# Optimization experiments

Measured on AMD Instinct MI355X. Metric: run time of the kernel, lower is better.

The kernel has to match this reference:

```python
import jax, jax.numpy as jnp
import numpy as np

D_MODEL = 1024
NUM_HEADS = 16
DEPTH = D_MODEL // NUM_HEADS
B, S = 2, 2048


def setup_inputs() -> dict:
    key = jax.random.key(0)
    ks = jax.random.split(key, 13)
    sc = 1.0 / np.sqrt(D_MODEL)
    inp = {
        "q": jax.random.normal(ks[0], (B, S, D_MODEL), jnp.float32),
        "k": jax.random.normal(ks[1], (B, S, D_MODEL), jnp.float32),
        "v": jax.random.normal(ks[2], (B, S, D_MODEL), jnp.float32),
        "mask": jax.random.randint(ks[3], (B, 1, S, S), 0, 2).astype(jnp.float32),
        "wq": jax.random.normal(ks[4], (D_MODEL, D_MODEL), jnp.float32) * sc,
        "bq": jnp.zeros((D_MODEL,), jnp.float32),
        "wk": jax.random.normal(ks[5], (D_MODEL, D_MODEL), jnp.float32) * sc,
        "bk": jnp.zeros((D_MODEL,), jnp.float32),
        "wv": jax.random.normal(ks[6], (D_MODEL, D_MODEL), jnp.float32) * sc,
        "bv": jnp.zeros((D_MODEL,), jnp.float32),
        "wo": jax.random.normal(ks[7], (D_MODEL, D_MODEL), jnp.float32) * sc,
        "bo": jnp.zeros((D_MODEL,), jnp.float32),
    }
    return inp


def _split_heads(x):
    # [B,S,D] -> [B,H,S,depth]
    b, s, _ = x.shape
    return x.reshape(b, s, NUM_HEADS, DEPTH).transpose(0, 2, 1, 3)


def reference(q, k, v, mask, wq, bq, wk, bk, wv, bv, wo, bo):
    qh = _split_heads(q @ wq.T + bq)
    kh = _split_heads(k @ wk.T + bk)
    vh = _split_heads(v @ wv.T + bv)
    logits = jnp.einsum("bhqd,bhkd->bhqk", qh, kh) / jnp.sqrt(
        jnp.asarray(DEPTH, jnp.float32))
    logits = logits + mask * (-1e9)
    attn = jax.nn.softmax(logits, axis=-1)
    out = jnp.einsum("bhqk,bhkd->bhqd", attn, vh)
    out = out.transpose(0, 2, 1, 3).reshape(q.shape[0], -1, D_MODEL)
    return out @ wo.T + bo
```

## Files before the change

kernel.cpp:

```cpp
#include <hip/hip_runtime.h>

#define D_MODEL 1024
#define NHEADS  16
#define DEPTH   64
#define BATCH   2
#define SEQ     2048
#define MROWS   (BATCH * SEQ)

typedef unsigned short u16;
typedef unsigned int   u32;
typedef unsigned long long u64;
typedef __bf16 bf16x8 __attribute__((ext_vector_type(8)));
typedef float  f32x4  __attribute__((ext_vector_type(4)));

__device__ __forceinline__ u16 f2b(float f) {
    return __builtin_bit_cast(u16, static_cast<__bf16>(f));
}
__device__ __forceinline__ bf16x8 ldb8(const u16* p) {
    return __builtin_bit_cast(bf16x8, *(const uint4*)p);
}

__global__ __launch_bounds__(256) void pack_mask(
    const float* __restrict__ mask, u64* __restrict__ bits)
{
    const int w    = blockIdx.x * 4 + (threadIdx.x >> 6);
    const int lane = threadIdx.x & 63;
    float m = mask[(size_t)w * 64 + lane];
    u64 b = __ballot(m > 0.5f);
    if (lane == 0) bits[w] = b;
}

__global__ __launch_bounds__(256, 3) void proj3(
    const float* __restrict__ q, const float* __restrict__ k, const float* __restrict__ v,
    const float* __restrict__ wq, const float* __restrict__ wk, const float* __restrict__ wv,
    const float* __restrict__ bq, const float* __restrict__ bk, const float* __restrict__ bv,
    u16* __restrict__ qws, u16* __restrict__ kws, u16* __restrict__ vtws)
{
    __shared__ __align__(16) u16 ldsA[128 * 40];
    __shared__ __align__(16) u16 ldsB[128 * 40];

    const int z = blockIdx.z;
    const float* X  = (z == 0) ? q  : (z == 1) ? k  : v;
    const float* W  = (z == 0) ? wq : (z == 1) ? wk : wv;
    const float* Bi = (z == 0) ? bq : (z == 1) ? bk : bv;
    u16* dst        = (z == 0) ? qws : (z == 1) ? kws : vtws;

    const int tid  = threadIdx.x;
    const int wv_  = tid >> 6;
    const int lane = tid & 63;
    const int quad = lane >> 4;
    const int l15  = lane & 15;
    const int bx = blockIdx.x, by = blockIdx.y;
    const int wm = (wv_ >> 1) * 64;
    const int wn = (wv_ & 1) * 64;

    f32x4 acc[4][4];
    for (int i = 0; i < 4; ++i)
        for (int j = 0; j < 4; ++j)
            acc[i][j] = (f32x4){0.f, 0.f, 0.f, 0.f};

    const int rowA0 = by * 128;
    const int rowB0 = bx * 128;

    const int sr = tid >> 3;
    const int sc = (tid & 7) * 4;

    float4 pa[4], pb[4];
    #pragma unroll
    for (int i = 0; i < 4; ++i) {
        pa[i] = *(const float4*)&X[(size_t)(rowA0 + sr + i * 32) * D_MODEL + sc];
        pb[i] = *(const float4*)&W[(size_t)(rowB0 + sr + i * 32) * D_MODEL + sc];
    }

    for (int it = 0; it < 32; ++it) {
        #pragma unroll
        for (int i = 0; i < 4; ++i) {
            ushort4 ha, hb;
            ha.x = f2b(pa[i].x); ha.y = f2b(pa[i].y); ha.z = f2b(pa[i].z); ha.w = f2b(pa[i].w);
            hb.x = f2b(pb[i].x); hb.y = f2b(pb[i].y); hb.z = f2b(pb[i].z); hb.w = f2b(pb[i].w);
            *(ushort4*)&ldsA[(sr + i * 32) * 40 + sc] = ha;
            *(ushort4*)&ldsB[(sr + i * 32) * 40 + sc] = hb;
        }
        __syncthreads();

        if (it < 31) {
            const int k0 = (it + 1) * 32;
            #pragma unroll
            for (int i = 0; i < 4; ++i) {
                pa[i] = *(const float4*)&X[(size_t)(rowA0 + sr + i * 32) * D_MODEL + k0 + sc];
                pb[i] = *(const float4*)&W[(size_t)(rowB0 + sr + i * 32) * D_MODEL + k0 + sc];
            }
        }

        bf16x8 af[4], bfr[4];
        #pragma unroll
        for (int t = 0; t < 4; ++t) {
            af[t]  = ldb8(&ldsA[(wm + t * 16 + l15) * 40 + quad * 8]);
            bfr[t] = ldb8(&ldsB[(wn + t * 16 + l15) * 40 + quad * 8]);
        }
        #pragma unroll
        for (int mt = 0; mt < 4; ++mt)
            #pragma unroll
            for (int nt = 0; nt < 4; ++nt)
                acc[mt][nt] = __builtin_amdgcn_mfma_f32_16x16x32_bf16(af[mt], bfr[nt], acc[mt][nt], 0, 0, 0);
        __syncthreads();
    }

    #pragma unroll
    for (int nt = 0; nt < 4; ++nt) {
        int n = bx * 128 + wn + nt * 16 + l15;
        float bvv = Bi[n];
        int h = n >> 6, d = n & 63;
        #pragma unroll
        for (int mt = 0; mt < 4; ++mt) {
            #pragma unroll
            for (int r = 0; r < 4; ++r) {
                int m = by * 128 + wm + mt * 16 + quad * 4 + r;
                float c = acc[mt][nt][r] + bvv;
                int b = m >> 11, s = m & (SEQ - 1);
                if (z != 2)
                    dst[(((size_t)(b * NHEADS + h) * SEQ) + s) * DEPTH + d] = f2b(c);
                else
                    dst[(((size_t)(b * NHEADS + h) * DEPTH) + d) * SEQ + s] = f2b(c);
            }
        }
    }
}

__global__ __launch_bounds__(256) void gemm_out(
    const u16* __restrict__ X, const float* __restrict__ W,
    const float* __restrict__ bias, float* __restrict__ out)
{
    __shared__ __align__(16) u16 ldsA[128 * 40];
    __shared__ __align__(16) u16 ldsB[64 * 40];

    const int tid  = threadIdx.x;
    const int wv_  = tid >> 6;
    const int lane = tid & 63;
    const int quad = lane >> 4;
    const int l15  = lane & 15;
    const int bx = blockIdx.x, by = blockIdx.y;
    const int wm = (wv_ >> 1) * 64;
    const int wn = (wv_ & 1) * 32;

    f32x4 acc[4][2];
    for (int i = 0; i < 4; ++i)
        for (int j = 0; j < 2; ++j)
            acc[i][j] = (f32x4){0.f, 0.f, 0.f, 0.f};

    const int rowA0 = by * 128;
    const int rowB0 = bx * 64;

    const int ar = tid >> 2, akc = (tid & 3) * 8;
    const int br = tid >> 3, bc = (tid & 7) * 4;

    uint4  paA[2];
    float4 paB[2];
    #pragma unroll
    for (int i = 0; i < 2; ++i) {
        paA[i] = *(const uint4*)&X[(size_t)(rowA0 + ar + i * 64) * D_MODEL + akc];
        paB[i] = *(const float4*)&W[(size_t)(rowB0 + br + i * 32) * D_MODEL + bc];
    }

    for (int it = 0; it < 32; ++it) {
        #pragma unroll
        for (int i = 0; i < 2; ++i) {
            *(uint4*)&ldsA[(ar + i * 64) * 40 + akc] = paA[i];
            ushort4 hb;
            hb.x = f2b(paB[i].x); hb.y = f2b(paB[i].y); hb.z = f2b(paB[i].z); hb.w = f2b(paB[i].w);
            *(ushort4*)&ldsB[(br + i * 32) * 40 + bc] = hb;
        }
        __syncthreads();

        if (it < 31) {
            const int k0 = (it + 1) * 32;
            #pragma unroll
            for (int i = 0; i < 2; ++i) {
                paA[i] = *(const uint4*)&X[(size_t)(rowA0 + ar + i * 64) * D_MODEL + k0 + akc];
                paB[i] = *(const float4*)&W[(size_t)(rowB0 + br + i * 32) * D_MODEL + k0 + bc];
            }
        }

        bf16x8 af[4], bfr[2];
        #pragma unroll
        for (int t = 0; t < 4; ++t)
            af[t] = ldb8(&ldsA[(wm + t * 16 + l15) * 40 + quad * 8]);
        #pragma unroll
        for (int t = 0; t < 2; ++t)
            bfr[t] = ldb8(&ldsB[(wn + t * 16 + l15) * 40 + quad * 8]);
        #pragma unroll
        for (int mt = 0; mt < 4; ++mt)
            #pragma unroll
            for (int nt = 0; nt < 2; ++nt)
                acc[mt][nt] = __builtin_amdgcn_mfma_f32_16x16x32_bf16(af[mt], bfr[nt], acc[mt][nt], 0, 0, 0);
        __syncthreads();
    }

    #pragma unroll
    for (int nt = 0; nt < 2; ++nt) {
        int n = bx * 64 + wn + nt * 16 + l15;
        float bvv = bias[n];
        #pragma unroll
        for (int mt = 0; mt < 4; ++mt) {
            #pragma unroll
            for (int r = 0; r < 4; ++r) {
                int m = by * 128 + wm + mt * 16 + quad * 4 + r;
                out[(size_t)m * D_MODEL + n] = acc[mt][nt][r] + bvv;
            }
        }
    }
}

__global__ __launch_bounds__(256, 3) void flash_attn(
    const u16* __restrict__ Q, const u16* __restrict__ K,
    const u16* __restrict__ Vt, const u64* __restrict__ maskbits,
    u16* __restrict__ O)
{
    __shared__ __align__(16) u16 ldsK[2][64 * 64];
    __shared__ __align__(16) u16 ldsV[2][64 * 64];
    __shared__ __align__(16) u16 ldsP[4][16 * 72];

    const int tid  = threadIdx.x;
    const int wv_  = tid >> 6;
    const int lane = tid & 63;
    const int quad = lane >> 4;
    const int l15  = lane & 15;
    const int bh = blockIdx.y;
    const int b  = bh >> 4, h = bh & 15;
    const int q0 = blockIdx.x * 64 + wv_ * 16;

    const u16* Qb = Q  + (size_t)bh * SEQ * DEPTH;
    const u16* Kb = K  + (size_t)bh * SEQ * DEPTH;
    const u16* Vb = Vt + (size_t)bh * DEPTH * SEQ;
    const u64* MB = maskbits + (size_t)b * SEQ * (SEQ / 64);

    const int srow = tid >> 3;
    const int sc8  = tid & 7;
    const int swz  = ((sc8 ^ (srow & 7)) * 8);
    const int kdst0 = srow * 64 + swz;
    const int kdst1 = (srow + 32) * 64 + swz;

    const int xk0 = ((quad ^ (l15 & 7)) * 8);
    const int xk1 = (((4 + quad) ^ (l15 & 7)) * 8);

    bf16x8 aq0 = ldb8(&Qb[(q0 + l15) * DEPTH + quad * 8]);
    bf16x8 aq1 = ldb8(&Qb[(q0 + l15) * DEPTH + 32 + quad * 8]);

    f32x4 oa[4];
    for (int i = 0; i < 4; ++i) oa[i] = (f32x4){0.f, 0.f, 0.f, 0.f};
    float lrow[4] = {0.f, 0.f, 0.f, 0.f};

    u16* myP = ldsP[wv_];

    uint4 kreg0 = *(const uint4*)&Kb[(size_t)srow * DEPTH + sc8 * 8];
    uint4 kreg1 = *(const uint4*)&Kb[(size_t)(srow + 32) * DEPTH + sc8 * 8];
    uint4 vreg0 = *(const uint4*)&Vb[(size_t)srow * SEQ + sc8 * 8];
    uint4 vreg1 = *(const uint4*)&Vb[(size_t)(srow + 32) * SEQ + sc8 * 8];

    for (int it = 0; it < 32; ++it) {
        const int buf = it & 1;
        u16* Kl = ldsK[buf];
        u16* Vl = ldsV[buf];

        *(uint4*)&Kl[kdst0] = kreg0;
        *(uint4*)&Kl[kdst1] = kreg1;
        *(uint4*)&Vl[kdst0] = vreg0;
        *(uint4*)&Vl[kdst1] = vreg1;
        __syncthreads();

        if (it < 31) {
            const int kb2 = (it + 1) * 64;
            kreg0 = *(const uint4*)&Kb[(size_t)(kb2 + srow) * DEPTH + sc8 * 8];
            kreg1 = *(const uint4*)&Kb[(size_t)(kb2 + srow + 32) * DEPTH + sc8 * 8];
            vreg0 = *(const uint4*)&Vb[(size_t)srow * SEQ + kb2 + sc8 * 8];
            vreg1 = *(const uint4*)&Vb[(size_t)(srow + 32) * SEQ + kb2 + sc8 * 8];
        }

        u64 mrow[4];
        #pragma unroll
        for (int r = 0; r < 4; ++r)
            mrow[r] = MB[(size_t)(q0 + quad * 4 + r) * (SEQ / 64) + it];

        #pragma unroll
        for (int cc = 0; cc < 4; ++cc) {
            const int row = cc * 16 + l15;
            bf16x8 bk0 = ldb8(&Kl[row * 64 + xk0]);
            bf16x8 bk1 = ldb8(&Kl[row * 64 + xk1]);
            f32x4 z = (f32x4){0.f, 0.f, 0.f, 0.f};
            z = __builtin_amdgcn_mfma_f32_16x16x32_bf16(aq0, bk0, z, 0, 0, 0);
            z = __builtin_amdgcn_mfma_f32_16x16x32_bf16(aq1, bk1, z, 0, 0, 0);
            #pragma unroll
            for (int r = 0; r < 4; ++r) {
                float e = __expf(z[r] * 0.125f);
                float p = ((mrow[r] >> (cc * 16 + l15)) & 1ull) ? 0.f : e;
                lrow[r] += p;
                myP[(quad * 4 + r) * 72 + cc * 16 + l15] = f2b(p);
            }
        }

        __builtin_amdgcn_wave_barrier();
        __builtin_amdgcn_s_waitcnt(0xc07f);
        __builtin_amdgcn_wave_barrier();
        bf16x8 pa0 = ldb8(&myP[l15 * 72 + quad * 8]);
        bf16x8 pa1 = ldb8(&myP[l15 * 72 + 32 + quad * 8]);

        #pragma unroll
        for (int n = 0; n < 4; ++n) {
            const int row = n * 16 + l15;
            bf16x8 bv0 = ldb8(&Vl[row * 64 + xk0]);
            bf16x8 bv1 = ldb8(&Vl[row * 64 + xk1]);
            oa[n] = __builtin_amdgcn_mfma_f32_16x16x32_bf16(pa0, bv0, oa[n], 0, 0, 0);
            oa[n] = __builtin_amdgcn_mfma_f32_16x16x32_bf16(pa1, bv1, oa[n], 0, 0, 0);
        }
    }

    #pragma unroll
    for (int r = 0; r < 4; ++r) {
        float s = lrow[r];
        #pragma unroll
        for (int off = 1; off < 16; off <<= 1)
            s += __shfl_xor(s, off, 64);
        lrow[r] = 1.0f / s;
    }
    #pragma unroll
    for (int n = 0; n < 4; ++n)
        #pragma unroll
        for (int r = 0; r < 4; ++r) {
            int m = q0 + quad * 4 + r;
            O[((size_t)b * SEQ + m) * D_MODEL + h * DEPTH + n * 16 + l15] =
                f2b(oa[n][r] * lrow[r]);
        }
}

extern "C" void kernel_launch(void* const* d_in, const int* in_sizes, int n_in,
                              void* d_out, int out_size, void* d_ws, size_t ws_size,
                              hipStream_t stream) {
    const float* q    = (const float*)d_in[0];
    const float* k    = (const float*)d_in[1];
    const float* v    = (const float*)d_in[2];
    const float* mask = (const float*)d_in[3];
    const float* wq   = (const float*)d_in[4];
    const float* bq   = (const float*)d_in[5];
    const float* wk   = (const float*)d_in[6];
    const float* bk   = (const float*)d_in[7];
    const float* wv   = (const float*)d_in[8];
    const float* bv   = (const float*)d_in[9];
    const float* wo   = (const float*)d_in[10];
    const float* bo   = (const float*)d_in[11];

    u16* base = (u16*)d_ws;
    const size_t seg = (size_t)BATCH * NHEADS * SEQ * DEPTH;
    u16* qws  = base;
    u16* kws  = base + seg;
    u16* vtws = base + 2 * seg;
    u16* ows  = base + 3 * seg;
    u64* mbits = (u64*)(base + 4 * seg);

    dim3 blk(256);
    hipLaunchKernelGGL(pack_mask, dim3(BATCH * SEQ * (SEQ / 64) / 4), blk, 0, stream, mask, mbits);

    dim3 gp(D_MODEL / 128, MROWS / 128, 3);
    hipLaunchKernelGGL(proj3, gp, blk, 0, stream,
                       q, k, v, wq, wk, wv, bq, bk, bv, qws, kws, vtws);

    dim3 ga(SEQ / 64, BATCH * NHEADS);
    hipLaunchKernelGGL(flash_attn, ga, blk, 0, stream, qws, kws, vtws, mbits, ows);

    dim3 go(D_MODEL / 64, MROWS / 128);
    hipLaunchKernelGGL(gemm_out, go, blk, 0, stream, ows, wo, bo, (float*)d_out);
}
```

Baseline: 335.9 us.

## Pre-convert inputs and weights to bf16, fold softmax scale into Q projection

Adds a conversion kernel that turns activations and all four weight matrices into bf16 up front, so the projection and output GEMMs load 16-bit data directly instead of converting fp32 to bf16 inside the inner loop. The softmax scale and log2(e) are folded into the Q projection so attention can use exp2f without a multiply. The per-lane mask bit extraction is simplified into 32-bit shifts. This costs an extra pass that reads and writes about 40 MB and needs more workspace, with an fp32 fallback when workspace is too small.

New measurement: 416.3 us. 1.24x slower.

```diff
diff --git a/kernel.cpp b/kernel.cpp
--- a/kernel.cpp
+++ b/kernel.cpp
@@ -6,6 +6,7 @@
 #define BATCH   2
 #define SEQ     2048
 #define MROWS   (BATCH * SEQ)
+#define QSCALE  0.18033688f
 
 typedef unsigned short u16;
 typedef unsigned int   u32;
@@ -30,9 +31,39 @@
     if (lane == 0) bits[w] = b;
 }
 
-__global__ __launch_bounds__(256, 3) void proj3(
-    const float* __restrict__ q, const float* __restrict__ k, const float* __restrict__ v,
+__global__ __launch_bounds__(256) void cvt_all(
+    const float* __restrict__ q,  const float* __restrict__ k,  const float* __restrict__ v,
     const float* __restrict__ wq, const float* __restrict__ wk, const float* __restrict__ wv,
+    const float* __restrict__ wo,
+    u16* __restrict__ qb, u16* __restrict__ kb, u16* __restrict__ vb,
+    u16* __restrict__ wqb, u16* __restrict__ wkb, u16* __restrict__ wvb,
+    u16* __restrict__ wob)
+{
+    const int blk = blockIdx.x;
+    const float* src; u16* dst; size_t base;
+    if (blk < 6144) {
+        int t = blk >> 11;
+        src = (t == 0) ? q : (t == 1) ? k : v;
+        dst = (t == 0) ? qb : (t == 1) ? kb : vb;
+        base = (size_t)(blk & 2047) * 2048;
+    } else {
+        int t = (blk - 6144) >> 9;
+        src = (t == 0) ? wq : (t == 1) ? wk : (t == 2) ? wv : wo;
+        dst = (t == 0) ? wqb : (t == 1) ? wkb : (t == 2) ? wvb : wob;
+        base = (size_t)((blk - 6144) & 511) * 2048;
+    }
+    size_t e = base + (size_t)threadIdx.x * 8;
+    float4 f0 = *(const float4*)&src[e];
+    float4 f1 = *(const float4*)&src[e + 4];
+    union { ushort s[8]; uint4 u; } o;
+    o.s[0] = f2b(f0.x); o.s[1] = f2b(f0.y); o.s[2] = f2b(f0.z); o.s[3] = f2b(f0.w);
+    o.s[4] = f2b(f1.x); o.s[5] = f2b(f1.y); o.s[6] = f2b(f1.z); o.s[7] = f2b(f1.w);
+    *(uint4*)&dst[e] = o.u;
+}
+
+__global__ __launch_bounds__(256, 3) void proj3_b(
+    const u16* __restrict__ xq, const u16* __restrict__ xk, const u16* __restrict__ xv,
+    const u16* __restrict__ wq, const u16* __restrict__ wk, const u16* __restrict__ wv,
     const float* __restrict__ bq, const float* __restrict__ bk, const float* __restrict__ bv,
     u16* __restrict__ qws, u16* __restrict__ kws, u16* __restrict__ vtws)
 {
@@ -40,8 +71,8 @@
     __shared__ __align__(16) u16 ldsB[128 * 40];
 
     const int z = blockIdx.z;
-    const float* X  = (z == 0) ? q  : (z == 1) ? k  : v;
-    const float* W  = (z == 0) ? wq : (z == 1) ? wk : wv;
+    const u16* X    = (z == 0) ? xq : (z == 1) ? xk : xv;
+    const u16* W    = (z == 0) ? wq : (z == 1) ? wk : wv;
     const float* Bi = (z == 0) ? bq : (z == 1) ? bk : bv;
     u16* dst        = (z == 0) ? qws : (z == 1) ? kws : vtws;
 
@@ -62,6 +93,101 @@
     const int rowA0 = by * 128;
     const int rowB0 = bx * 128;
 
+    const int sr = tid >> 2;
+    const int sc = (tid & 3) * 8;
+
+    uint4 pA[2], pB[2];
+    #pragma unroll
+    for (int i = 0; i < 2; ++i) {
+        pA[i] = *(const uint4*)&X[(size_t)(rowA0 + sr + i * 64) * D_MODEL + sc];
+        pB[i] = *(const uint4*)&W[(size_t)(rowB0 + sr + i * 64) * D_MODEL + sc];
+    }
+
+    for (int it = 0; it < 32; ++it) {
+        #pragma unroll
+        for (int i = 0; i < 2; ++i) {
+            *(uint4*)&ldsA[(sr + i * 64) * 40 + sc] = pA[i];
+            *(uint4*)&ldsB[(sr + i * 64) * 40 + sc] = pB[i];
+        }
+        __syncthreads();
+
+        if (it < 31) {
+            const int k0 = (it + 1) * 32;
+            #pragma unroll
+            for (int i = 0; i < 2; ++i) {
+                pA[i] = *(const uint4*)&X[(size_t)(rowA0 + sr + i * 64) * D_MODEL + k0 + sc];
+                pB[i] = *(const uint4*)&W[(size_t)(rowB0 + sr + i * 64) * D_MODEL + k0 + sc];
+            }
+        }
+
+        bf16x8 af[4], bfr[4];
+        #pragma unroll
+        for (int t = 0; t < 4; ++t) {
+            af[t]  = ldb8(&ldsA[(wm + t * 16 + l15) * 40 + quad * 8]);
+            bfr[t] = ldb8(&ldsB[(wn + t * 16 + l15) * 40 + quad * 8]);
+        }
+        #pragma unroll
+        for (int mt = 0; mt < 4; ++mt)
+            #pragma unroll
+            for (int nt = 0; nt < 4; ++nt)
+                acc[mt][nt] = __builtin_amdgcn_mfma_f32_16x16x32_bf16(af[mt], bfr[nt], acc[mt][nt], 0, 0, 0);
+        __syncthreads();
+    }
+
+    #pragma unroll
+    for (int nt = 0; nt < 4; ++nt) {
+        int n = bx * 128 + wn + nt * 16 + l15;
+        float bvv = Bi[n];
+        int h = n >> 6, d = n & 63;
+        #pragma unroll
+        for (int mt = 0; mt < 4; ++mt) {
+            #pragma unroll
+            for (int r = 0; r < 4; ++r) {
+                int m = by * 128 + wm + mt * 16 + quad * 4 + r;
+                float c = acc[mt][nt][r] + bvv;
+                if (z == 0) c *= QSCALE;
+                int b = m >> 11, s = m & (SEQ - 1);
+                if (z != 2)
+                    dst[(((size_t)(b * NHEADS + h) * SEQ) + s) * DEPTH + d] = f2b(c);
+                else
+                    dst[(((size_t)(b * NHEADS + h) * DEPTH) + d) * SEQ + s] = f2b(c);
+            }
+        }
+    }
+}
+
+__global__ __launch_bounds__(256, 3) void proj3_f(
+    const float* __restrict__ q, const float* __restrict__ k, const float* __restrict__ v,
+    const float* __restrict__ wq, const float* __restrict__ wk, const float* __restrict__ wv,
+    const float* __restrict__ bq, const float* __restrict__ bk, const float* __restrict__ bv,
+    u16* __restrict__ qws, u16* __restrict__ kws, u16* __restrict__ vtws)
+{
+    __shared__ __align__(16) u16 ldsA[128 * 40];
+    __shared__ __align__(16) u16 ldsB[128 * 40];
+
+    const int z = blockIdx.z;
+    const float* X  = (z == 0) ? q  : (z == 1) ? k  : v;
+    const float* W  = (z == 0) ? wq : (z == 1) ? wk : wv;
+    const float* Bi = (z == 0) ? bq : (z == 1) ? bk : bv;
+    u16* dst        = (z == 0) ? qws : (z == 1) ? kws : vtws;
+
+    const int tid  = threadIdx.x;
+    const int wv_  = tid >> 6;
+    const int lane = tid & 63;
+    const int quad = lane >> 4;
+    const int l15  = lane & 15;
+    const int bx = blockIdx.x, by = blockIdx.y;
+    const int wm = (wv_ >> 1) * 64;
+    const int wn = (wv_ & 1) * 64;
+
+    f32x4 acc[4][4];
+    for (int i = 0; i < 4; ++i)
+        for (int j = 0; j < 4; ++j)
+            acc[i][j] = (f32x4){0.f, 0.f, 0.f, 0.f};
+
+    const int rowA0 = by * 128;
+    const int rowB0 = bx * 128;
+
     const int sr = tid >> 3;
     const int sc = (tid & 7) * 4;
 
@@ -117,6 +243,7 @@
             for (int r = 0; r < 4; ++r) {
                 int m = by * 128 + wm + mt * 16 + quad * 4 + r;
                 float c = acc[mt][nt][r] + bvv;
+                if (z == 0) c *= QSCALE;
                 int b = m >> 11, s = m & (SEQ - 1);
                 if (z != 2)
                     dst[(((size_t)(b * NHEADS + h) * SEQ) + s) * DEPTH + d] = f2b(c);
@@ -127,8 +254,9 @@
     }
 }
 
-__global__ __launch_bounds__(256) void gemm_out(
-    const u16* __restrict__ X, const float* __restrict__ W,
+template <bool W_BF16>
+__global__ __launch_bounds__(256) void gemm_out_t(
+    const u16* __restrict__ X, const void* __restrict__ Wv,
     const float* __restrict__ bias, float* __restrict__ out)
 {
     __shared__ __align__(16) u16 ldsA[128 * 40];
@@ -153,31 +281,50 @@
 
     const int ar = tid >> 2, akc = (tid & 3) * 8;
     const int br = tid >> 3, bc = (tid & 7) * 4;
+    const int ubr = tid >> 2, ubc = (tid & 3) * 8;
 
     uint4  paA[2];
-    float4 paB[2];
-    #pragma unroll
-    for (int i = 0; i < 2; ++i) {
+    float4 paBf[2];
+    uint4  paBb;
+    #pragma unroll
+    for (int i = 0; i < 2; ++i)
         paA[i] = *(const uint4*)&X[(size_t)(rowA0 + ar + i * 64) * D_MODEL + akc];
-        paB[i] = *(const float4*)&W[(size_t)(rowB0 + br + i * 32) * D_MODEL + bc];
+    if (W_BF16) {
+        paBb = *(const uint4*)&((const u16*)Wv)[(size_t)(rowB0 + ubr) * D_MODEL + ubc];
+    } else {
+        #pragma unroll
+        for (int i = 0; i < 2; ++i)
+            paBf[i] = *(const float4*)&((const float*)Wv)[(size_t)(rowB0 + br + i * 32) * D_MODEL + bc];
     }
 
     for (int it = 0; it < 32; ++it) {
         #pragma unroll
-        for (int i = 0; i < 2; ++i) {
+        for (int i = 0; i < 2; ++i)
             *(uint4*)&ldsA[(ar + i * 64) * 40 + akc] = paA[i];
-            ushort4 hb;
-            hb.x = f2b(paB[i].x); hb.y = f2b(paB[i].y); hb.z = f2b(paB[i].z); hb.w = f2b(paB[i].w);
-            *(ushort4*)&ldsB[(br + i * 32) * 40 + bc] = hb;
+        if (W_BF16) {
+            *(uint4*)&ldsB[ubr * 40 + ubc] = paBb;
+        } else {
+            #pragma unroll
+            for (int i = 0; i < 2; ++i) {
+                ushort4 hb;
+                hb.x = f2b(paBf[i].x); hb.y = f2b(paBf[i].y);
+                hb.z = f2b(paBf[i].z); hb.w = f2b(paBf[i].w);
+                *(ushort4*)&ldsB[(br + i * 32) * 40 + bc] = hb;
+            }
         }
         __syncthreads();
 
         if (it < 31) {
             const int k0 = (it + 1) * 32;
             #pragma unroll
-            for (int i = 0; i < 2; ++i) {
+            for (int i = 0; i < 2; ++i)
                 paA[i] = *(const uint4*)&X[(size_t)(rowA0 + ar + i * 64) * D_MODEL + k0 + akc];
-                paB[i] = *(const float4*)&W[(size_t)(rowB0 + br + i * 32) * D_MODEL + k0 + bc];
+            if (W_BF16) {
+                paBb = *(const uint4*)&((const u16*)Wv)[(size_t)(rowB0 + ubr) * D_MODEL + k0 + ubc];
+            } else {
+                #pragma unroll
+                for (int i = 0; i < 2; ++i)
+                    paBf[i] = *(const float4*)&((const float*)Wv)[(size_t)(rowB0 + br + i * 32) * D_MODEL + k0 + bc];
             }
         }
 
@@ -276,10 +423,13 @@
             vreg1 = *(const uint4*)&Vb[(size_t)(srow + 32) * SEQ + kb2 + sc8 * 8];
         }
 
-        u64 mrow[4];
-        #pragma unroll
-        for (int r = 0; r < 4; ++r)
-            mrow[r] = MB[(size_t)(q0 + quad * 4 + r) * (SEQ / 64) + it];
+        u32 tlo[4], thi[4];
+        #pragma unroll
+        for (int r = 0; r < 4; ++r) {
+            u64 t = MB[(size_t)(q0 + quad * 4 + r) * (SEQ / 64) + it] >> l15;
+            tlo[r] = (u32)t;
+            thi[r] = (u32)(t >> 32);
+        }
 
         #pragma unroll
         for (int cc = 0; cc < 4; ++cc) {
@@ -291,8 +441,10 @@
             z = __builtin_amdgcn_mfma_f32_16x16x32_bf16(aq1, bk1, z, 0, 0, 0);
             #pragma unroll
             for (int r = 0; r < 4; ++r) {
-                float e = __expf(z[r] * 0.125f);
-                float p = ((mrow[r] >> (cc * 16 + l15)) & 1ull) ? 0.f : e;
+                u32 w   = (cc < 2) ? tlo[r] : thi[r];
+                u32 bit = (cc & 1) ? ((w >> 16) & 1u) : (w & 1u);
+                float e = exp2f(z[r]);
+                float p = bit ? 0.f : e;
                 lrow[r] += p;
                 myP[(quad * 4 + r) * 72 + cc * 16 + l15] = f2b(p);
             }
@@ -350,22 +502,45 @@
 
     u16* base = (u16*)d_ws;
     const size_t seg = (size_t)BATCH * NHEADS * SEQ * DEPTH;
+    const size_t wseg = (size_t)D_MODEL * D_MODEL;
     u16* qws  = base;
     u16* kws  = base + seg;
     u16* vtws = base + 2 * seg;
     u16* ows  = base + 3 * seg;
-    u64* mbits = (u64*)(base + 4 * seg);
+
+    const size_t needA = (7 * seg + 4 * wseg) * 2 + (size_t)BATCH * SEQ * (SEQ / 64) * 8;
+    const bool tierA = ws_size >= needA;
 
     dim3 blk(256);
-    hipLaunchKernelGGL(pack_mask, dim3(BATCH * SEQ * (SEQ / 64) / 4), blk, 0, stream, mask, mbits);
-
     dim3 gp(D_MODEL / 128, MROWS / 128, 3);
-    hipLaunchKernelGGL(proj3, gp, blk, 0, stream,
-                       q, k, v, wq, wk, wv, bq, bk, bv, qws, kws, vtws);
-
     dim3 ga(SEQ / 64, BATCH * NHEADS);
-    hipLaunchKernelGGL(flash_attn, ga, blk, 0, stream, qws, kws, vtws, mbits, ows);
-
     dim3 go(D_MODEL / 64, MROWS / 128);
-    hipLaunchKernelGGL(gemm_out, go, blk, 0, stream, ows, wo, bo, (float*)d_out);
-}
+
+    if (tierA) {
+        u16* qb  = base + 4 * seg;
+        u16* kb  = base + 5 * seg;
+        u16* vb  = base + 6 * seg;
+        u16* wqb = base + 7 * seg;
+        u16* wkb = wqb + wseg;
+        u16* wvb = wkb + wseg;
+        u16* wob = wvb + wseg;
+        u64* mbits = (u64*)(wob + wseg);
+
+        hipLaunchKernelGGL(cvt_all, dim3(8192), blk, 0, stream,
+                           q, k, v, wq, wk, wv, wo, qb, kb, vb, wqb, wkb, wvb, wob);
+        hipLaunchKernelGGL(pack_mask, dim3(BATCH * SEQ * (SEQ / 64) / 4), blk, 0, stream, mask, mbits);
+        hipLaunchKernelGGL(proj3_b, gp, blk, 0, stream,
+                           qb, kb, vb, wqb, wkb, wvb, bq, bk, bv, qws, kws, vtws);
+        hipLaunchKernelGGL(flash_attn, ga, blk, 0, stream, qws, kws, vtws, mbits, ows);
+        hipLaunchKernelGGL((gemm_out_t<true>), go, blk, 0, stream,
+                           ows, (const void*)wob, bo, (float*)d_out);
+    } else {
+        u64* mbits = (u64*)(base + 4 * seg);
+        hipLaunchKernelGGL(pack_mask, dim3(BATCH * SEQ * (SEQ / 64) / 4), blk, 0, stream, mask, mbits);
+        hipLaunchKernelGGL(proj3_f, gp, blk, 0, stream,
+                           q, k, v, wq, wk, wv, bq, bk, bv, qws, kws, vtws);
+        hipLaunchKernelGGL(flash_attn, ga, blk, 0, stream, qws, kws, vtws, mbits, ows);
+        hipLaunchKernelGGL((gemm_out_t<false>), go, blk, 0, stream,
+                           ows, (const void*)wo, bo, (float*)d_out);
+    }
+}
```
